# Optimization experiments

Measured on AMD Instinct MI355X. Metric: run time of the kernel, lower is better.

The kernel has to match this reference:

```python
import jax, jax.numpy as jnp
import numpy as np

D = 128       # embedding_dim
BC = 64       # block_count
BS = 512      # block_size
K = 6         # main conv kernel size
OV = 2 * BC   # overlap_size
SCALE = 1.0 / np.sqrt(D).astype(np.float32)


def setup_inputs() -> dict:
    key = jax.random.key(0)
    ks = jax.random.split(key, 6)
    B = 8
    x = jax.random.normal(ks[0], (B, BC * BS, D), dtype=jnp.float32)
    w_lw = jax.random.normal(ks[1], (D, 1), dtype=jnp.float32) * 0.05
    b_lw = jnp.zeros((1,), dtype=jnp.float32)
    conv_w = jax.random.normal(ks[2], (D, D, K), dtype=jnp.float32) * 0.05  # (out, in, k)
    conv_b = jnp.zeros((D,), dtype=jnp.float32)
    fusion_w = jax.random.normal(ks[3], (3 * D, D), dtype=jnp.float32) * 0.05
    fusion_b = jnp.zeros((D,), dtype=jnp.float32)
    return {"x": x, "w_lw": w_lw, "b_lw": b_lw, "conv_w": conv_w,
            "conv_b": conv_b, "fusion_w": fusion_w, "fusion_b": fusion_b}


def _prefix_softmax_weighted_sum(x, logits):
    # x: (B, L, D), logits: (B, L) -- faithful replica of the torch scan
    pmax = jax.lax.cummax(logits, axis=1)
    ex = jnp.exp(logits - pmax)                    # (B, L)
    psum = jnp.cumsum(ex, axis=1)                  # (B, L)
    wpre = jnp.cumsum(ex[..., None] * x, axis=1)   # (B, L, D)
    return wpre / psum[..., None]


def _attn(q, k, v):
    # q: (N, 1, D); k, v: (N, S, D)
    s = jnp.einsum('nqd,nkd->nqk', q, k) * SCALE
    return jnp.einsum('nqk,nkd->nqd', jax.nn.softmax(s, axis=-1), v)


def reference(x, w_lw, b_lw, conv_w, conv_b, fusion_w, fusion_b):
    B, L, _ = x.shape  # L == BC * BS, so F.pad in the original is a no-op
    logits = jax.nn.silu(x @ w_lw + b_lw)[..., 0]          # (B, L)
    prefix_x = _prefix_softmax_weighted_sum(x, logits) + x  # (B, L, D)

    # per-block conv1d (kernel 6, padding='same' in torch => pad (2,3))
    blocks = prefix_x.reshape(B * BC, BS, D).transpose(0, 2, 1)  # (N, D, BS)
    conv = jax.lax.conv_general_dilated(
        blocks, conv_w, window_strides=(1,), padding=[(2, 3)],
        dimension_numbers=('NCH', 'OIH', 'NCH')) + conv_b[None, :, None]
    blocks_c = conv.transpose(0, 2, 1)                           # (N, BS, D)
    block_repr = jnp.max(blocks_c, axis=1)[:, None, :]           # (N, 1, D)

    # overlap windows: replicate-pad end by OV//2, slice, gather OV-wide windows
    xov = jnp.pad(prefix_x, ((0, 0), (0, OV // 2), (0, 0)), mode='edge')
    xov = xov[:, BS - OV // 2:, :]                               # (B, (BC-1)*BS + OV, D)
    idx = (jnp.arange(BC) * BS)[:, None] + jnp.arange(OV)[None, :]  # (BC, OV)
    xbo = xov[:, idx, :].reshape(B * BC, OV, D)

    a_s = _attn(block_repr, blocks_c, blocks_c)  # block->self
    a_o = _attn(block_repr, xbo, xbo)            # block->overlap
    fused = jnp.concatenate([a_s, a_o, block_repr], axis=-1)    # (N, 1, 3D)
    out = (fused @ fusion_w + fusion_b).reshape(B, BC, D)
    return (out, out)
```

## Files before the change

### kernel.cpp

```cpp
#include <hip/hip_runtime.h>
#include <hip/hip_bf16.h>

#define NB 8
#define LSEQ 32768
#define DCH 128
#define NCHUNK 1024
#define NSUB 4096
#define NBLK 512
#define PH 520
#define SCALE_F 0.08838834764831845f

typedef __bf16 bf16x8 __attribute__((ext_vector_type(8)));
typedef float f32x4 __attribute__((ext_vector_type(4)));

__device__ __forceinline__ float bf2f(unsigned short u) {
    return __uint_as_float(((unsigned)u) << 16);
}
__device__ __forceinline__ unsigned short f2bf(float f) {
    unsigned u = __float_as_uint(f);
    u += 0x7fffu + ((u >> 16) & 1u);
    return (unsigned short)(u >> 16);
}

__device__ __forceinline__ void async_copy16(const void* gsrc, void* ldst) {
    __builtin_amdgcn_global_load_lds(
        (const __attribute__((address_space(1))) unsigned int*)gsrc,
        (__attribute__((address_space(3))) unsigned int*)ldst, 16, 0, 0);
}

__global__ __launch_bounds__(256) void k_logits2(const float* __restrict__ x,
                                                 const float* __restrict__ w_lw,
                                                 const float* __restrict__ b_lw,
                                                 float* __restrict__ logits,
                                                 float* __restrict__ subM) {
    int chunk = blockIdx.x, t = threadIdx.x;
    int g = t & 15, rs = t >> 4;
    __shared__ float sp[256 * 17];
    __shared__ float red[256];
    float wv[8];
    #pragma unroll
    for (int e = 0; e < 8; ++e) wv[e] = w_lw[g * 8 + e];
    float bb = b_lw[0];
    size_t base = (size_t)chunk * 256 * DCH;
    for (int i = 0; i < 16; ++i) {
        int row = rs * 16 + i;
        float4 a  = *(const float4*)(x + base + (size_t)row * DCH + g * 8);
        float4 b4 = *(const float4*)(x + base + (size_t)row * DCH + g * 8 + 4);
        sp[row * 17 + g] = a.x * wv[0] + a.y * wv[1] + a.z * wv[2] + a.w * wv[3] +
                           b4.x * wv[4] + b4.y * wv[5] + b4.z * wv[6] + b4.w * wv[7];
    }
    __syncthreads();
    float s = bb;
    #pragma unroll
    for (int j = 0; j < 16; ++j) s += sp[t * 17 + j];
    float l = s / (1.f + expf(-s));
    logits[(size_t)chunk * 256 + t] = l;
    red[t] = l;
    __syncthreads();
    for (int off = 32; off >= 1; off >>= 1) {
        if ((t & 63) < off) red[t] = fmaxf(red[t], red[t + off]);
        __syncthreads();
    }
    if ((t & 63) == 0) subM[chunk * 4 + (t >> 6)] = red[t];
}

__global__ __launch_bounds__(64) void k_seed_max2(const float* __restrict__ subM,
                                                  float* __restrict__ seedM) {
    int b = blockIdx.x, lane = threadIdx.x;
    const float* src = subM + b * 512;
    float* dst = seedM + b * 512;
    float v[8];
    float m = -INFINITY;
    #pragma unroll
    for (int j = 0; j < 8; ++j) { v[j] = src[lane * 8 + j]; m = fmaxf(m, v[j]); }
    float incl = m;
    #pragma unroll
    for (int off = 1; off < 64; off <<= 1) {
        float o = __shfl_up(incl, off, 64);
        if (lane >= off) incl = fmaxf(incl, o);
    }
    float ex = __shfl_up(incl, 1, 64);
    if (lane == 0) ex = -INFINITY;
    float run = ex;
    #pragma unroll
    for (int j = 0; j < 8; ++j) { dst[lane * 8 + j] = run; run = fmaxf(run, v[j]); }
}

__global__ __launch_bounds__(256) void k_sums(const float* __restrict__ x,
                                              const float* __restrict__ logits,
                                              const float* __restrict__ seedM,
                                              float* __restrict__ exg,
                                              float* __restrict__ S_w,
                                              float* __restrict__ S_wx) {
    int chunk = blockIdx.x, t = threadIdx.x;
    int g = t & 15, rs = t >> 4;
    __shared__ float llog[256];
    __shared__ float wbuf[256];
    __shared__ float red[256];
    __shared__ float rp[16 * 130];
    llog[t] = logits[(size_t)chunk * 256 + t];
    __syncthreads();
    if (t < 4) {
        float M = seedM[chunk * 4 + t];
        float m = -INFINITY;
        for (int i = 0; i < 64; ++i) {
            float l = llog[t * 64 + i];
            m = fmaxf(m, l);
            wbuf[t * 64 + i] = expf(l - fmaxf(M, m));
        }
    }
    __syncthreads();
    float w_t = wbuf[t];
    exg[(size_t)chunk * 256 + t] = w_t;
    red[t] = w_t;
    __syncthreads();
    for (int off = 32; off >= 1; off >>= 1) {
        if ((t & 63) < off) red[t] += red[t + off];
        __syncthreads();
    }
    if ((t & 63) == 0) S_w[chunk * 4 + (t >> 6)] = red[t];
    float acc[8];
    #pragma unroll
    for (int e = 0; e < 8; ++e) acc[e] = 0.f;
    size_t base = (size_t)chunk * 256 * DCH;
    for (int i = 0; i < 16; ++i) {
        int row = rs * 16 + i;
        float w = wbuf[row];
        float4 a  = *(const float4*)(x + base + (size_t)row * DCH + g * 8);
        float4 b4 = *(const float4*)(x + base + (size_t)row * DCH + g * 8 + 4);
        acc[0] += w * a.x;  acc[1] += w * a.y;  acc[2] += w * a.z;  acc[3] += w * a.w;
        acc[4] += w * b4.x; acc[5] += w * b4.y; acc[6] += w * b4.z; acc[7] += w * b4.w;
    }
    #pragma unroll
    for (int e = 0; e < 8; ++e) rp[rs * 130 + g * 8 + e] = acc[e];
    __syncthreads();
    #pragma unroll
    for (int k = 0; k < 2; ++k) {
        int idx = k * 256 + t;
        int sub = idx >> 7, c = idx & 127;
        float sm = rp[(sub * 4 + 0) * 130 + c] + rp[(sub * 4 + 1) * 130 + c] +
                   rp[(sub * 4 + 2) * 130 + c] + rp[(sub * 4 + 3) * 130 + c];
        S_wx[((size_t)chunk * 4 + sub) * DCH + c] = sm;
    }
}

__global__ __launch_bounds__(64) void k_seed_w(const float* __restrict__ S_w,
                                               float* __restrict__ sS_w) {
    int b = blockIdx.x, lane = threadIdx.x;
    const float* src = S_w + b * 512;
    float* dst = sS_w + b * 512;
    float v[8];
    float tot = 0.f;
    #pragma unroll
    for (int j = 0; j < 8; ++j) { v[j] = src[lane * 8 + j]; tot += v[j]; }
    float incl = tot;
    #pragma unroll
    for (int off = 1; off < 64; off <<= 1) {
        float o = __shfl_up(incl, off, 64);
        if (lane >= off) incl += o;
    }
    float ex = __shfl_up(incl, 1, 64);
    if (lane == 0) ex = 0.f;
    float run = ex;
    #pragma unroll
    for (int j = 0; j < 8; ++j) { dst[lane * 8 + j] = run; run += v[j]; }
}

__global__ __launch_bounds__(256) void k_seed_sums2(const float* __restrict__ S_wx,
                                                    float* __restrict__ sS_wx) {
    int b = blockIdx.x >> 3, cg = blockIdx.x & 7;
    int t = threadIdx.x;
    int cl = t & 15, seg = t >> 4;
    int c = cg * 16 + cl;
    __shared__ float tots[16][17];
    const float* src = S_wx + (size_t)b * 512 * DCH + c;
    float* dst = sS_wx + (size_t)b * 512 * DCH + c;
    int s0 = seg * 32;
    float tot = 0.f;
    for (int j = 0; j < 32; ++j) tot += src[(size_t)(s0 + j) * DCH];
    tots[seg][cl] = tot;
    __syncthreads();
    if (t < 16) {
        float run = 0.f;
        for (int s = 0; s < 16; ++s) { float tmp = tots[s][t]; tots[s][t] = run; run += tmp; }
    }
    __syncthreads();
    float run = tots[seg][cl];
    for (int j = 0; j < 32; ++j) {
        float val = src[(size_t)(s0 + j) * DCH];
        dst[(size_t)(s0 + j) * DCH] = run;
        run += val;
    }
}

__global__ __launch_bounds__(256) void k_init(const float* __restrict__ conv_w,
                                              unsigned short* __restrict__ W3,
                                              unsigned short* __restrict__ P) {
    int n = blockIdx.x, t = threadIdx.x;
    for (int i = t; i < 1024; i += 256) {
        int rr = i >> 7;
        int row = (rr < 2) ? rr : 512 + rr;
        P[(n * PH + row) * DCH + (i & 127)] = 0;
    }
    int idx = n * 256 + t;
    if (idx < 98304) {
        int e  = idx & 7;
        int o  = (idx >> 3) & 127;
        int kc = (idx >> 10) & 3;
        int kt2 = idx >> 12;
        int kt = kt2 >> 1, ks = kt2 & 1;
        int i  = (kt & 1) * 64 + (ks * 4 + kc) * 8 + e;
        int kn = kt >> 1;
        W3[idx] = f2bf(conv_w[(o * 128 + i) * 6 + kn]);
    }
}

__global__ __launch_bounds__(128) void k_apply(const float* __restrict__ x,
                                               const float* __restrict__ exg,
                                               const float* __restrict__ sS_w,
                                               const float* __restrict__ sS_wx,
                                               unsigned short* __restrict__ P) {
    int t = threadIdx.x, w = t >> 6, lane = t & 63;
    int s = blockIdx.x * 2 + w;
    int b = s >> 9, sb = s & 511;
    __shared__ float e2[128];
    e2[t] = exg[(size_t)blockIdx.x * 128 + t];
    float2 axx = *(const float2*)(sS_wx + (size_t)s * DCH + 2 * lane);
    float aex = sS_w[s];
    __syncthreads();
    const float* es = e2 + w * 64;
    int pib0 = sb * 64;
    int n = b * 64 + (pib0 >> 9);
    int row0 = (pib0 & 511) + 2;
    const float* xp = x + ((size_t)b * LSEQ + pib0) * DCH + 2 * lane;
    unsigned short* pp = P + ((size_t)n * PH + row0) * DCH + 2 * lane;
    for (int j = 0; j < 64; ++j) {
        float e = es[j];
        aex += e;
        float2 xv = *(const float2*)xp;
        axx.x += e * xv.x;
        axx.y += e * xv.y;
        float inv = 1.f / aex;
        unsigned pk = ((unsigned)f2bf(axx.y * inv + xv.y) << 16) | f2bf(axx.x * inv + xv.x);
        *(unsigned*)pp = pk;
        xp += DCH;
        pp += DCH;
    }
}

__global__ __launch_bounds__(256) void k_conv(const unsigned short* __restrict__ P,
                                              const unsigned short* __restrict__ W3,
                                              const float* __restrict__ conv_b,
                                              unsigned short* __restrict__ convout) {
    int n = blockIdx.x >> 2;
    int h0 = (blockIdx.x & 3) * 128;
    __shared__ __align__(16) unsigned short lds[128 * 136];
    char* abuf0 = (char*)lds;
    char* abuf1 = (char*)lds + 16384;
    int t = threadIdx.x;
    int wave = t >> 6, lane = t & 63;
    f32x4 acc[4][4] = {};
    const unsigned short* Pn = P + (size_t)n * PH * DCH;
    int wm = (wave >> 1) * 64, wn = (wave & 1) * 64;
    int cpos = lane & 7;
    int kchunk = lane >> 4;
    int bcol = wn + (lane & 15);

    bf16x8 breg[2][8];

    auto stageA = [&](int kt, char* dst) {
        int kn = kt >> 1, c0 = (kt & 1) * 64;
        #pragma unroll
        for (int j = 0; j < 4; ++j) {
            int r = (wave * 4 + j) * 8 + (lane >> 3);
            int gr = h0 + kn + r;
            int csrcA = cpos ^ (gr & 7);
            async_copy16(Pn + (size_t)gr * DCH + c0 + csrcA * 8,
                         dst + (wave * 4 + j) * 1024 + lane * 16);
        }
    };
    auto loadB = [&](int kt, bf16x8* dstB) {
        #pragma unroll
        for (int ks = 0; ks < 2; ++ks)
            #pragma unroll
            for (int ni = 0; ni < 4; ++ni)
                dstB[ks * 4 + ni] = *(const bf16x8*)(
                    W3 + (size_t)((kt * 2 + ks) * 4 + kchunk) * 1024 + (bcol + ni * 16) * 8);
    };

    stageA(0, abuf0);
    loadB(0, breg[0]);
    __syncthreads();

    #pragma unroll
    for (int kt = 0; kt < 12; ++kt) {
        char* cbuf = (kt & 1) ? abuf1 : abuf0;
        if (kt < 11) {
            stageA(kt + 1, (kt & 1) ? abuf0 : abuf1);
            loadB(kt + 1, breg[(kt + 1) & 1]);
        }
        int kn = kt >> 1;
        #pragma unroll
        for (int ks = 0; ks < 2; ++ks) {
            bf16x8 af[4];
            #pragma unroll
            for (int mi = 0; mi < 4; ++mi) {
                int rA = wm + mi * 16 + (lane & 15);
                int pA = (ks * 4 + kchunk) ^ ((kn + rA) & 7);
                af[mi] = *(const bf16x8*)(cbuf + rA * 128 + pA * 16);
            }
            #pragma unroll
            for (int mi = 0; mi < 4; ++mi)
                #pragma unroll
                for (int ni = 0; ni < 4; ++ni)
                    acc[mi][ni] = __builtin_amdgcn_mfma_f32_16x16x32_bf16(af[mi],
                                                                          breg[kt & 1][ks * 4 + ni],
                                                                          acc[mi][ni], 0, 0, 0);
        }
        __syncthreads();
    }
    #pragma unroll
    for (int mi = 0; mi < 4; ++mi)
        #pragma unroll
        for (int ni = 0; ni < 4; ++ni) {
            int col = wn + ni * 16 + (lane & 15);
            float bias = conv_b[col];
            #pragma unroll
            for (int r = 0; r < 4; ++r) {
                int row = wm + mi * 16 + (lane >> 4) * 4 + r;
                lds[row * 136 + col] = f2bf(acc[mi][ni][r] + bias);
            }
        }
    __syncthreads();
    size_t base = (size_t)(n * 512 + h0) * DCH;
    #pragma unroll
    for (int it = 0; it < 8; ++it) {
        int idx = it * 256 + t;
        int row = idx >> 4, g = idx & 15;
        uint4 v = *(const uint4*)(lds + row * 136 + g * 8);
        *(uint4*)(convout + base + (size_t)row * DCH + g * 8) = v;
    }
}

__global__ __launch_bounds__(256) void k_tail(const unsigned short* __restrict__ conv,
                                              const unsigned short* __restrict__ P,
                                              const float* __restrict__ fusion_w,
                                              const float* __restrict__ fusion_b,
                                              float* __restrict__ block_repr,
                                              float* __restrict__ out) {
    int n = blockIdx.x, t = threadIdx.x;
    int g = t & 15, rs = t >> 4;
    int b = n >> 6, c = n & 63;
    __shared__ __align__(16) float sp[512 * 17];
    __shared__ float s[512];
    __shared__ float br[128];
    __shared__ float as_l[128];
    __shared__ float ao_l[128];
    __shared__ float red[128];
    __shared__ int rb[128];
    float* rp = sp;
    const unsigned short* base = conv + (size_t)n * 512 * DCH;

    float m[8];
    #pragma unroll
    for (int e = 0; e < 8; ++e) m[e] = -INFINITY;
    for (int i = 0; i < 32; ++i) {
        int row = i * 16 + rs;
        uint4 v = *(const uint4*)(base + row * DCH + g * 8);
        unsigned vv[4] = {v.x, v.y, v.z, v.w};
        #pragma unroll
        for (int e = 0; e < 4; ++e) {
            m[2 * e]     = fmaxf(m[2 * e],     bf2f((unsigned short)(vv[e] & 0xffff)));
            m[2 * e + 1] = fmaxf(m[2 * e + 1], bf2f((unsigned short)(vv[e] >> 16)));
        }
    }
    #pragma unroll
    for (int e = 0; e < 8; ++e) rp[rs * 130 + g * 8 + e] = m[e];
    __syncthreads();
    if (t < 128) {
        float bm = rp[t];
        #pragma unroll
        for (int r2 = 1; r2 < 16; ++r2) bm = fmaxf(bm, rp[r2 * 130 + t]);
        br[t] = bm;
        block_repr[n * DCH + t] = bm;
    }
    __syncthreads();

    float brv[8];
    #pragma unroll
    for (int e = 0; e < 8; ++e) brv[e] = br[g * 8 + e];
    for (int i = 0; i < 32; ++i) {
        int row = i * 16 + rs;
        uint4 v = *(const uint4*)(base + row * DCH + g * 8);
        unsigned vv[4] = {v.x, v.y, v.z, v.w};
        float p = 0.f;
        #pragma unroll
        for (int e = 0; e < 4; ++e) {
            p += bf2f((unsigned short)(vv[e] & 0xffff)) * brv[2 * e];
            p += bf2f((unsigned short)(vv[e] >> 16))    * brv[2 * e + 1];
        }
        sp[row * 17 + g] = p;
    }
    __syncthreads();
    #pragma unroll
    for (int rr = 0; rr < 2; ++rr) {
        int row = t * 2 + rr;
        float p = 0.f;
        #pragma unroll
        for (int j = 0; j < 16; ++j) p += sp[row * 17 + j];
        s[row] = p * SCALE_F;
    }
    __syncthreads();

    float* redA = sp;
    float mm = fmaxf(s[t], s[t + 256]);
    __syncthreads();
    redA[t] = mm;
    __syncthreads();
    for (int off = 128; off > 0; off >>= 1) {
        if (t < off) redA[t] = fmaxf(redA[t], redA[t + off]);
        __syncthreads();
    }
    float smax = redA[0];
    __syncthreads();
    float e0 = expf(s[t] - smax), e1 = expf(s[t + 256] - smax);
    redA[t] = e0 + e1;
    __syncthreads();
    for (int off = 128; off > 0; off >>= 1) {
        if (t < off) redA[t] += redA[t + off];
        __syncthreads();
    }
    float inv = 1.f / redA[0];
    __syncthreads();
    s[t] = e0 * inv;
    s[t + 256] = e1 * inv;
    __syncthreads();

    float acc[8];
    #pragma unroll
    for (int e = 0; e < 8; ++e) acc[e] = 0.f;
    for (int i = 0; i < 32; ++i) {
        int row = i * 16 + rs;
        float w = s[row];
        uint4 v = *(const uint4*)(base + row * DCH + g * 8);
        unsigned vv[4] = {v.x, v.y, v.z, v.w};
        #pragma unroll
        for (int e = 0; e < 4; ++e) {
            acc[2 * e]     += w * bf2f((unsigned short)(vv[e] & 0xffff));
            acc[2 * e + 1] += w * bf2f((unsigned short)(vv[e] >> 16));
        }
    }
    #pragma unroll
    for (int e = 0; e < 8; ++e) rp[rs * 130 + g * 8 + e] = acc[e];
    __syncthreads();
    if (t < 128) {
        float p = 0.f;
        #pragma unroll
        for (int r2 = 0; r2 < 16; ++r2) p += rp[r2 * 130 + t];
        as_l[t] = p;
    }

    if (t < 128) {
        int pib = (c + 1) * 512 - 64 + t;
        pib = min(pib, LSEQ - 1);
        int n2 = b * 64 + (pib >> 9);
        int row = (pib & 511) + 2;
        rb[t] = (n2 * PH + row) * DCH;
    }
    __syncthreads();
    #pragma unroll
    for (int r = 0; r < 8; ++r) {
        int row = rs * 8 + r;
        uint4 v = *(const uint4*)(P + rb[row] + g * 8);
        unsigned vv[4] = {v.x, v.y, v.z, v.w};
        float p = 0.f;
        #pragma unroll
        for (int e = 0; e < 4; ++e) {
            p += bf2f((unsigned short)(vv[e] & 0xffff)) * brv[2 * e];
            p += bf2f((unsigned short)(vv[e] >> 16))    * brv[2 * e + 1];
        }
        sp[row * 17 + g] = p;
    }
    __syncthreads();
    if (t < 128) {
        float p = 0.f;
        #pragma unroll
        for (int j = 0; j < 16; ++j) p += sp[t * 17 + j];
        s[t] = p * SCALE_F;
        red[t] = s[t];
    }
    __syncthreads();
    for (int off = 64; off > 0; off >>= 1) {
        if (t < off) red[t] = fmaxf(red[t], red[t + off]);
        __syncthreads();
    }
    float smaxB = red[0];
    __syncthreads();
    if (t < 128) {
        float e = expf(s[t] - smaxB);
        s[t] = e;
        red[t] = e;
    }
    __syncthreads();
    for (int off = 64; off > 0; off >>= 1) {
        if (t < off) red[t] += red[t + off];
        __syncthreads();
    }
    float invB = 1.f / red[0];
    __syncthreads();
    if (t < 128) s[t] *= invB;
    __syncthreads();
    float accB[8];
    #pragma unroll
    for (int e = 0; e < 8; ++e) accB[e] = 0.f;
    #pragma unroll
    for (int r = 0; r < 8; ++r) {
        int row = rs * 8 + r;
        float w = s[row];
        uint4 v = *(const uint4*)(P + rb[row] + g * 8);
        unsigned vv[4] = {v.x, v.y, v.z, v.w};
        #pragma unroll
        for (int e = 0; e < 4; ++e) {
            accB[2 * e]     += w * bf2f((unsigned short)(vv[e] & 0xffff));
            accB[2 * e + 1] += w * bf2f((unsigned short)(vv[e] >> 16));
        }
    }
    #pragma unroll
    for (int e = 0; e < 8; ++e) sp[rs * 130 + g * 8 + e] = accB[e];
    __syncthreads();
    if (t < 128) {
        float p = 0.f;
        #pragma unroll
        for (int r2 = 0; r2 < 16; ++r2) p += sp[r2 * 130 + t];
        ao_l[t] = p;
    }
    __syncthreads();

    float* fu = sp + 8320;
    if (t < 128) {
        fu[t] = as_l[t];
        fu[128 + t] = ao_l[t];
        fu[256 + t] = br[t];
    }
    __syncthreads();
    {
        int col = t & 127, h = t >> 7;
        float a2 = (h == 0) ? fusion_b[col] : 0.f;
        for (int j = h * 192; j < h * 192 + 192; ++j)
            a2 += fu[j] * fusion_w[j * DCH + col];
        sp[h * 128 + col] = a2;
    }
    __syncthreads();
    if (t < 128) {
        float v = sp[t] + sp[128 + t];
        out[n * DCH + t] = v;
        out[NB * 64 * DCH + n * DCH + t] = v;
    }
}

extern "C" void kernel_launch(void* const* d_in, const int* in_sizes, int n_in,
                              void* d_out, int out_size, void* d_ws, size_t ws_size,
                              hipStream_t stream) {
    const float* x        = (const float*)d_in[0];
    const float* w_lw     = (const float*)d_in[1];
    const float* b_lw     = (const float*)d_in[2];
    const float* conv_w   = (const float*)d_in[3];
    const float* conv_b   = (const float*)d_in[4];
    const float* fusion_w = (const float*)d_in[5];
    const float* fusion_b = (const float*)d_in[6];
    float* out = (float*)d_out;

    char* ws = (char*)d_ws;
    size_t off = 0;
    auto alloc = [&](size_t bytes) { char* p = ws + off; off += (bytes + 255) & ~(size_t)255; return p; };
    float* logits     = (float*)alloc(NB * LSEQ * 4);
    float* exg        = (float*)alloc(NB * LSEQ * 4);
    float* subM       = (float*)alloc(NSUB * 4);
    float* seedM      = (float*)alloc(NSUB * 4);
    float* S_w        = (float*)alloc(NSUB * 4);
    float* sS_w       = (float*)alloc(NSUB * 4);
    float* S_wx       = (float*)alloc((size_t)NSUB * DCH * 4);
    float* sS_wx      = (float*)alloc((size_t)NSUB * DCH * 4);
    float* block_repr = (float*)alloc(NBLK * DCH * 4);
    unsigned short* W3      = (unsigned short*)alloc(128 * 768 * 2);
    unsigned short* P       = (unsigned short*)alloc((size_t)NBLK * PH * DCH * 2);
    unsigned short* convout = (unsigned short*)alloc((size_t)NBLK * 512 * DCH * 2);

    k_init<<<NBLK, 256, 0, stream>>>(conv_w, W3, P);
    k_logits2<<<NCHUNK, 256, 0, stream>>>(x, w_lw, b_lw, logits, subM);
    k_seed_max2<<<NB, 64, 0, stream>>>(subM, seedM);
    k_sums<<<NCHUNK, 256, 0, stream>>>(x, logits, seedM, exg, S_w, S_wx);
    k_seed_w<<<NB, 64, 0, stream>>>(S_w, sS_w);
    k_seed_sums2<<<NB * 8, 256, 0, stream>>>(S_wx, sS_wx);
    k_apply<<<NSUB / 2, 128, 0, stream>>>(x, exg, sS_w, sS_wx, P);
    k_conv<<<NBLK * 4, 256, 0, stream>>>(P, W3, conv_b, convout);
    k_tail<<<NBLK, 256, 0, stream>>>(convout, P, fusion_w, fusion_b, block_repr, out);
}
```

Before: 363.3 us.

## Stage full conv input panel once in LDS instead of per-tap double buffering

The conv kernel now loads a 144x128 bf16 panel (the 128 output rows plus halo) into LDS in a single up-front pass and reads each of the 6 kernel taps as a shifted row offset, rather than re-staging a 128x64 A tile for each of the 12 k-steps through a double buffer. This removes about 6x redundant global/async loads of overlapping rows and the per-iteration __syncthreads. In exchange, LDS use rises to 36 KB per block, which may reduce occupancy, and there is no longer any overlap between A loading and compute.

```diff
diff --git a/kernel.cpp b/kernel.cpp
--- a/kernel.cpp
+++ b/kernel.cpp
@@ -254,31 +254,17 @@
                                               unsigned short* __restrict__ convout) {
     int n = blockIdx.x >> 2;
     int h0 = (blockIdx.x & 3) * 128;
-    __shared__ __align__(16) unsigned short lds[128 * 136];
-    char* abuf0 = (char*)lds;
-    char* abuf1 = (char*)lds + 16384;
+    __shared__ __align__(16) char panel[144 * 256];
     int t = threadIdx.x;
     int wave = t >> 6, lane = t & 63;
     f32x4 acc[4][4] = {};
     const unsigned short* Pn = P + (size_t)n * PH * DCH;
     int wm = (wave >> 1) * 64, wn = (wave & 1) * 64;
-    int cpos = lane & 7;
     int kchunk = lane >> 4;
     int bcol = wn + (lane & 15);
 
     bf16x8 breg[2][8];
 
-    auto stageA = [&](int kt, char* dst) {
-        int kn = kt >> 1, c0 = (kt & 1) * 64;
-        #pragma unroll
-        for (int j = 0; j < 4; ++j) {
-            int r = (wave * 4 + j) * 8 + (lane >> 3);
-            int gr = h0 + kn + r;
-            int csrcA = cpos ^ (gr & 7);
-            async_copy16(Pn + (size_t)gr * DCH + c0 + csrcA * 8,
-                         dst + (wave * 4 + j) * 1024 + lane * 16);
-        }
-    };
     auto loadB = [&](int kt, bf16x8* dstB) {
         #pragma unroll
         for (int ks = 0; ks < 2; ++ks)
@@ -288,26 +274,34 @@
                     W3 + (size_t)((kt * 2 + ks) * 4 + kchunk) * 1024 + (bcol + ni * 16) * 8);
     };
 
-    stageA(0, abuf0);
+    {
+        int c = lane & 15;
+        #pragma unroll
+        for (int j = 0; j < 9; ++j) {
+            int r = j * 16 + wave * 4 + (lane >> 4);
+            int gr = h0 + r;
+            int grc = min(gr, PH - 1);
+            int srcc = (c & 8) | ((c & 7) ^ (gr & 7));
+            async_copy16(Pn + (size_t)grc * DCH + srcc * 8,
+                         panel + j * 4096 + wave * 1024 + lane * 16);
+        }
+    }
     loadB(0, breg[0]);
     __syncthreads();
 
     #pragma unroll
     for (int kt = 0; kt < 12; ++kt) {
-        char* cbuf = (kt & 1) ? abuf1 : abuf0;
-        if (kt < 11) {
-            stageA(kt + 1, (kt & 1) ? abuf0 : abuf1);
-            loadB(kt + 1, breg[(kt + 1) & 1]);
-        }
+        if (kt < 11) loadB(kt + 1, breg[(kt + 1) & 1]);
         int kn = kt >> 1;
+        int cb = (kt & 1) * 8;
         #pragma unroll
         for (int ks = 0; ks < 2; ++ks) {
             bf16x8 af[4];
             #pragma unroll
             for (int mi = 0; mi < 4; ++mi) {
-                int rA = wm + mi * 16 + (lane & 15);
-                int pA = (ks * 4 + kchunk) ^ ((kn + rA) & 7);
-                af[mi] = *(const bf16x8*)(cbuf + rA * 128 + pA * 16);
+                int row = wm + mi * 16 + (lane & 15) + kn;
+                int phys = cb + ((ks * 4 + kchunk) ^ ((h0 + row) & 7));
+                af[mi] = *(const bf16x8*)(panel + row * 256 + phys * 16);
             }
             #pragma unroll
             for (int mi = 0; mi < 4; ++mi)
@@ -317,8 +311,9 @@
                                                                           breg[kt & 1][ks * 4 + ni],
                                                                           acc[mi][ni], 0, 0, 0);
         }
-        __syncthreads();
-    }
+    }
+    __syncthreads();
+    unsigned short* clds = (unsigned short*)panel;
     #pragma unroll
     for (int mi = 0; mi < 4; ++mi)
         #pragma unroll
@@ -328,7 +323,7 @@
             #pragma unroll
             for (int r = 0; r < 4; ++r) {
                 int row = wm + mi * 16 + (lane >> 4) * 4 + r;
-                lds[row * 136 + col] = f2bf(acc[mi][ni][r] + bias);
+                clds[row * 136 + col] = f2bf(acc[mi][ni][r] + bias);
             }
         }
     __syncthreads();
@@ -337,7 +332,7 @@
     for (int it = 0; it < 8; ++it) {
         int idx = it * 256 + t;
         int row = idx >> 4, g = idx & 15;
-        uint4 v = *(const uint4*)(lds + row * 136 + g * 8);
+        uint4 v = *(const uint4*)(clds + row * 136 + g * 8);
         *(uint4*)(convout + base + (size_t)row * DCH + g * 8) = v;
     }
 }
```

New measurement: 353.4 us. 2.7% less time.
